# Kernel tuning notes

Hardware: AMD Instinct MI355X
Metric: run time of the kernel (lower is better)

The kernel has to match this reference:

```python
import jax, jax.numpy as jnp
import numpy as np

ATT_HEADS = 4
H_FEATS = 16
IN_FEATS = 64
N_NODES = 50000
N_EDGES = 1000000


def setup_inputs() -> dict:
    key = jax.random.key(0)
    ks = jax.random.split(key, 12)
    h = jax.random.normal(ks[0], (N_NODES, IN_FEATS), dtype=jnp.float32)
    src_idx = jax.random.randint(ks[1], (N_EDGES,), 0, N_NODES)
    dst_idx = jax.random.randint(ks[2], (N_EDGES,), 0, N_NODES)
    s = 1.0 / np.sqrt(IN_FEATS)
    # w_liner: Linear(in_feats, h_feats*att_heads)
    W_w = jax.random.uniform(ks[3], (IN_FEATS, H_FEATS * ATT_HEADS), jnp.float32, -s, s)
    b_w = jax.random.uniform(ks[4], (H_FEATS * ATT_HEADS,), jnp.float32, -s, s)
    # atten: Linear(2*h_feats, 1)
    sa = 1.0 / np.sqrt(2 * H_FEATS)
    W_a = jax.random.uniform(ks[5], (2 * H_FEATS, 1), jnp.float32, -sa, sa)
    b_a = jax.random.uniform(ks[6], (1,), jnp.float32, -sa, sa)
    # relation_aware: d_liner Linear(in_feats, in_feats), f_liner Linear(3*in_feats, 1)
    W_d = jax.random.uniform(ks[7], (IN_FEATS, IN_FEATS), jnp.float32, -s, s)
    b_d = jax.random.uniform(ks[8], (IN_FEATS,), jnp.float32, -s, s)
    sf = 1.0 / np.sqrt(3 * IN_FEATS)
    W_f = jax.random.uniform(ks[9], (3 * IN_FEATS, 1), jnp.float32, -sf, sf)
    b_f = jax.random.uniform(ks[10], (1,), jnp.float32, -sf, sf)
    return {"h": h, "src_idx": src_idx, "dst_idx": dst_idx,
            "W_w": W_w, "b_w": b_w, "W_a": W_a, "b_a": b_a,
            "W_d": W_d, "b_d": b_d, "W_f": W_f, "b_f": b_f}


def reference(h, src_idx, dst_idx, W_w, b_w, W_a, b_a, W_d, b_d, W_f, b_f):
    N = h.shape[0]
    # sign_edges: relation_aware score -> sign per edge
    s_feat = h[src_idx] @ W_d + b_d            # [E, F]
    d_feat = h[dst_idx] @ W_d + b_d            # [E, F]
    e_feat = jnp.concatenate([s_feat, d_feat, s_feat - d_feat], axis=-1)
    score = jnp.tanh(e_feat @ W_f + b_f)[:, 0]  # [E]
    sign = jnp.sign(score)
    # node transform
    hp = h @ W_w + b_w                          # [N, H*hf]
    # message: signed src features, per-head concat with dst, attention logit
    sf = (sign[:, None] * hp[src_idx]).reshape(-1, ATT_HEADS, H_FEATS)  # [E,H,hf]
    df = hp[dst_idx].reshape(-1, ATT_HEADS, H_FEATS)                    # [E,H,hf]
    z = jnp.concatenate([sf, df], axis=-1)                              # [E,H,2hf]
    alpha = jax.nn.leaky_relu(z @ W_a + b_a)                            # [E,H,1]
    # reduce: segment softmax over incoming edges of each dst node
    amax = jax.ops.segment_max(alpha, dst_idx, num_segments=N)          # [N,H,1]
    ex = jnp.exp(alpha - amax[dst_idx])
    esum = jax.ops.segment_sum(ex, dst_idx, num_segments=N)             # [N,H,1]
    w = ex / esum[dst_idx]                                              # [E,H,1]
    out = jax.ops.segment_sum(w * sf, dst_idx, num_segments=N)          # [N,H,hf]
    return out.reshape(N, ATT_HEADS * H_FEATS)
```

## Files before the change

### kernel.cpp

```cpp
#include <hip/hip_runtime.h>
#include <hip/hip_fp16.h>

constexpr int F  = 64;
constexpr int HEADS = 4;
constexpr int CAP = 256;

__global__ __launch_bounds__(256) void node_kernel(
    const float* __restrict__ h,
    const float* __restrict__ W_w, const float* __restrict__ b_w,
    const float* __restrict__ W_a,
    const float* __restrict__ W_d, const float* __restrict__ b_d,
    const float* __restrict__ W_f,
    float* __restrict__ tfeat, __half* __restrict__ hp,
    double* __restrict__ u_arr, double* __restrict__ v_arr,
    float* __restrict__ a_src, float* __restrict__ a_dst,
    unsigned* __restrict__ cnt, int N, int nb)
{
    __shared__ float sWT[F * F];
    __shared__ float sb[F];
    __shared__ double swfA[F], swfB[F];
    __shared__ float sWa[32];

    int tid = threadIdx.x;
    bool isW = blockIdx.x >= nb;
    const float* Wsrc = isW ? W_w : W_d;
    for (int i = tid; i < F * F; i += 256) {
        int k = i >> 6, j = i & 63;
        sWT[j * F + k] = Wsrc[i];
    }
    if (tid < F) sb[tid] = isW ? b_w[tid] : b_d[tid];
    if (!isW && tid < F) {
        swfA[tid] = (double)W_f[tid] + (double)W_f[2 * F + tid];
        swfB[tid] = (double)W_f[F + tid] - (double)W_f[2 * F + tid];
    }
    if (isW && tid < 32) sWa[tid] = W_a[tid];
    __syncthreads();

    int blk = isW ? (blockIdx.x - nb) : blockIdx.x;
    int n = blk * 256 + tid;
    if (n >= N) return;

    if (!isW) cnt[n] = 0;

    float4 hv[16];
    const float4* h4 = reinterpret_cast<const float4*>(h + (size_t)n * F);
#pragma unroll
    for (int i = 0; i < 16; i++) hv[i] = h4[i];

    if (!isW) {
        double u = 0.0, v = 0.0;
        float4 tq;
        float4* trow = reinterpret_cast<float4*>(tfeat + (size_t)n * F);
#pragma unroll 4
        for (int j = 0; j < F; j++) {
            const float4* row = reinterpret_cast<const float4*>(&sWT[j * F]);
            float t = 0.f;
#pragma unroll
            for (int kk = 0; kk < 16; kk++) {
                float4 w = row[kk];
                float4 x = hv[kk];
                t = fmaf(x.x, w.x, t);
                t = fmaf(x.y, w.y, t);
                t = fmaf(x.z, w.z, t);
                t = fmaf(x.w, w.w, t);
            }
            t = t + sb[j];
            u = fma((double)t, swfA[j], u);
            v = fma((double)t, swfB[j], v);
            if ((j & 3) == 0) tq.x = t;
            else if ((j & 3) == 1) tq.y = t;
            else if ((j & 3) == 2) tq.z = t;
            else { tq.w = t; trow[j >> 2] = tq; }
        }
        u_arr[n] = u;
        v_arr[n] = v;
    } else {
        __half2* prow = reinterpret_cast<__half2*>(hp + (size_t)n * F);
#pragma unroll
        for (int qh = 0; qh < 4; qh++) {
            float asq = 0.f, adq = 0.f;
            float pprev = 0.f;
#pragma unroll 4
            for (int jj = 0; jj < 16; jj++) {
                int j = qh * 16 + jj;
                const float4* row = reinterpret_cast<const float4*>(&sWT[j * F]);
                float p = 0.f;
#pragma unroll
                for (int kk = 0; kk < 16; kk++) {
                    float4 w = row[kk];
                    float4 x = hv[kk];
                    p = fmaf(x.x, w.x, p);
                    p = fmaf(x.y, w.y, p);
                    p = fmaf(x.z, w.z, p);
                    p = fmaf(x.w, w.w, p);
                }
                p = p + sb[j];
                asq = fmaf(p, sWa[jj], asq);
                adq = fmaf(p, sWa[16 + jj], adq);
                if ((jj & 1) == 0) pprev = p;
                else prow[j >> 1] = __floats2half2_rn(pprev, p);
            }
            a_src[n * HEADS + qh] = asq;
            a_dst[n * HEADS + qh] = adq;
        }
    }
}

__device__ __noinline__ float tier2_sign(
    const float* __restrict__ tfeat, const float* __restrict__ sWf,
    int s, int d, float bf)
{
    const float4* ts = reinterpret_cast<const float4*>(tfeat + (size_t)s * F);
    const float4* td = reinterpret_cast<const float4*>(tfeat + (size_t)d * F);
    float sv[F];
#pragma unroll
    for (int i = 0; i < 16; i++) {
        float4 a = ts[i];
        sv[4 * i + 0] = a.x; sv[4 * i + 1] = a.y;
        sv[4 * i + 2] = a.z; sv[4 * i + 3] = a.w;
    }
    float acc = 0.f;
#pragma unroll
    for (int j = 0; j < F; j++) acc = fmaf(sv[j], sWf[j], acc);
#pragma unroll
    for (int i = 0; i < 16; i++) {
        float4 a = td[i];
        acc = fmaf(a.x, sWf[F + 4 * i + 0], acc);
        acc = fmaf(a.y, sWf[F + 4 * i + 1], acc);
        acc = fmaf(a.z, sWf[F + 4 * i + 2], acc);
        acc = fmaf(a.w, sWf[F + 4 * i + 3], acc);
    }
#pragma unroll
    for (int i = 0; i < 16; i++) {
        float4 a = td[i];
        acc = fmaf(sv[4 * i + 0] - a.x, sWf[2 * F + 4 * i + 0], acc);
        acc = fmaf(sv[4 * i + 1] - a.y, sWf[2 * F + 4 * i + 1], acc);
        acc = fmaf(sv[4 * i + 2] - a.z, sWf[2 * F + 4 * i + 2], acc);
        acc = fmaf(sv[4 * i + 3] - a.w, sWf[2 * F + 4 * i + 3], acc);
    }
    float sp = acc + bf;
    return (sp > 0.f) ? 1.f : (sp < 0.f ? -1.f : 0.f);
}

__global__ __launch_bounds__(256) void count_sign_kernel(
    const int* __restrict__ src_idx, const int* __restrict__ dst_idx,
    const double* __restrict__ u_arr, const double* __restrict__ v_arr,
    const float* __restrict__ tfeat, const float* __restrict__ W_f,
    const float* __restrict__ b_f,
    unsigned* __restrict__ cnt, unsigned* __restrict__ pc, int E)
{
    __shared__ float sWf[3 * F];
    int tid = threadIdx.x;
    if (tid < 3 * F) sWf[tid] = W_f[tid];
    __syncthreads();

    float bf = b_f[0];
    int e0 = blockIdx.x * 512 + tid;
    int e1 = e0 + 256;
    bool ok0 = e0 < E, ok1 = e1 < E;

    int s0 = 0, d0 = 0, s1 = 0, d1 = 0;
    if (ok0) { s0 = src_idx[e0]; d0 = dst_idx[e0]; }
    if (ok1) { s1 = src_idx[e1]; d1 = dst_idx[e1]; }

    unsigned p0 = ok0 ? atomicAdd(&cnt[d0], 1u) : 0u;
    unsigned p1 = ok1 ? atomicAdd(&cnt[d1], 1u) : 0u;

    double us0 = ok0 ? u_arr[s0] : 0.0, vd0 = ok0 ? v_arr[d0] : 0.0;
    double us1 = ok1 ? u_arr[s1] : 0.0, vd1 = ok1 ? v_arr[d1] : 0.0;
    double m0 = us0 + vd0 + (double)bf;
    double m1 = us1 + vd1 + (double)bf;

    float sg0 = (fabs(m0) >= 1e-4) ? ((m0 > 0.0) ? 1.f : -1.f)
                                   : (ok0 ? tier2_sign(tfeat, sWf, s0, d0, bf) : 0.f);
    float sg1 = (fabs(m1) >= 1e-4) ? ((m1 > 0.0) ? 1.f : -1.f)
                                   : (ok1 ? tier2_sign(tfeat, sWf, s1, d1, bf) : 0.f);

    if (ok0) {
        unsigned c0 = (sg0 > 0.f) ? 0u : (sg0 < 0.f ? 1u : 2u);
        pc[e0] = p0 | (c0 << 30);
    }
    if (ok1) {
        unsigned c1 = (sg1 > 0.f) ? 0u : (sg1 < 0.f ? 1u : 2u);
        pc[e1] = p1 | (c1 << 30);
    }
}

__global__ __launch_bounds__(256) void scan1_kernel(
    const unsigned* __restrict__ cnt, unsigned* __restrict__ rowptr,
    unsigned* __restrict__ bsum, int N)
{
    int t = threadIdx.x;
    int i = blockIdx.x * 256 + t;
    unsigned v = (i < N) ? cnt[i] : 0u;
    unsigned x = v;
#pragma unroll
    for (int off = 1; off < 64; off <<= 1) {
        unsigned y = __shfl_up(x, off);
        if ((t & 63) >= off) x += y;
    }
    __shared__ unsigned wsum[4];
    if ((t & 63) == 63) wsum[t >> 6] = x;
    __syncthreads();
    unsigned pre = 0;
#pragma unroll
    for (int w = 0; w < 3; w++) if (w < (t >> 6)) pre += wsum[w];
    unsigned incl = x + pre;
    if (i < N) rowptr[i] = incl - v;
    if (t == 255) bsum[blockIdx.x] = incl;
}

__global__ __launch_bounds__(256) void scan3_kernel(
    unsigned* __restrict__ rowptr, const unsigned* __restrict__ bsum,
    int N, int E, int nb)
{
    int t = threadIdx.x;
    int lim = min((int)blockIdx.x, nb);
    unsigned v = 0;
    for (int w = t; w < lim; w += 256) v += bsum[w];
#pragma unroll
    for (int off = 32; off >= 1; off >>= 1) v += __shfl_xor(v, off);
    __shared__ unsigned ws[4];
    if ((t & 63) == 0) ws[t >> 6] = v;
    __syncthreads();
    unsigned prefix = ws[0] + ws[1] + ws[2] + ws[3];

    int i = blockIdx.x * 256 + t;
    if (i < N) rowptr[i] += prefix;
    if (i == 0) rowptr[N] = (unsigned)E;
}

__global__ __launch_bounds__(256) void place_kernel(
    const int* __restrict__ src_idx, const int* __restrict__ dst_idx,
    const unsigned* __restrict__ pc, const unsigned* __restrict__ rowptr,
    unsigned* __restrict__ src_packed, int E)
{
    int e = blockIdx.x * 256 + threadIdx.x;
    if (e >= E) return;
    unsigned p = pc[e];
    unsigned pos = p & 0x3FFFFFFFu;
    unsigned code = p & 0xC0000000u;
    int d = dst_idx[e];
    src_packed[rowptr[d] + pos] = (unsigned)src_idx[e] | code;
}

__global__ __launch_bounds__(256) void dst_gather_kernel(
    const unsigned* __restrict__ rowptr,
    const unsigned* __restrict__ src_packed,
    const float* __restrict__ a_src, const float* __restrict__ a_dst,
    const float* __restrict__ b_a,
    const __half* __restrict__ hp,
    float* __restrict__ out, int N)
{
    __shared__ float sw[4][CAP * 4];
    __shared__ unsigned ssrc[4][CAP];

    int tid = threadIdx.x;
    int wslot = tid >> 6;
    int lane = tid & 63;
    int q = lane >> 4;
    int d = (blockIdx.x * 256 + tid) >> 6;
    bool valid = d < N;

    unsigned start = 0, end = 0;
    float ba = b_a[0];
    float4 ad4 = make_float4(0.f, 0.f, 0.f, 0.f);
    if (valid) {
        start = rowptr[d];
        end = rowptr[d + 1];
        ad4 = *reinterpret_cast<const float4*>(a_dst + (size_t)d * HEADS);
    }
    float adq = (q == 0) ? ad4.x : (q == 1) ? ad4.y : (q == 2) ? ad4.z : ad4.w;

    float4 p = make_float4(0.f, 0.f, 0.f, 0.f);
    if (valid) {
        for (unsigned i = start + lane; i < end; i += 64) {
            unsigned sp = src_packed[i];
            unsigned s = sp & 0x3FFFFFFFu;
            unsigned c = sp >> 30;
            float sgn = (c == 0u) ? 1.f : (c == 1u ? -1.f : 0.f);
            float4 as4 = *reinterpret_cast<const float4*>(a_src + (size_t)s * HEADS);
            float ap0 = fmaf(sgn, as4.x, ad4.x) + ba;
            float ap1 = fmaf(sgn, as4.y, ad4.y) + ba;
            float ap2 = fmaf(sgn, as4.z, ad4.z) + ba;
            float ap3 = fmaf(sgn, as4.w, ad4.w) + ba;
            float e0 = expf(ap0 > 0.f ? ap0 : 0.01f * ap0);
            float e1 = expf(ap1 > 0.f ? ap1 : 0.01f * ap1);
            float e2 = expf(ap2 > 0.f ? ap2 : 0.01f * ap2);
            float e3 = expf(ap3 > 0.f ? ap3 : 0.01f * ap3);
            p.x += e0; p.y += e1; p.z += e2; p.w += e3;
            unsigned slot = i - start;
            if (slot < CAP) {
                *reinterpret_cast<float4*>(&sw[wslot][slot * 4]) =
                    make_float4(sgn * e0, sgn * e1, sgn * e2, sgn * e3);
                ssrc[wslot][slot] = s;
            }
        }
    }
    __syncthreads();

#pragma unroll
    for (int off = 32; off >= 1; off >>= 1) {
        p.x += __shfl_xor(p.x, off);
        p.y += __shfl_xor(p.y, off);
        p.z += __shfl_xor(p.z, off);
        p.w += __shfl_xor(p.w, off);
    }
    if (!valid) return;

    float esq = (q == 0) ? p.x : (q == 1) ? p.y : (q == 2) ? p.z : p.w;
    float rinv = (end > start) ? (1.0f / esq) : 0.f;

    const float* swb = &sw[wslot][0];
    const unsigned* ssb = &ssrc[wslot][0];
    unsigned cend = min(end, start + CAP);
    unsigned cnt_c = cend - start;

    float a0 = 0.f, a1 = 0.f, a2 = 0.f, a3 = 0.f;
    unsigned t0 = 0;
    for (; t0 + 8 <= cnt_c; t0 += 8) {
        float w0 = swb[(t0 + 0) * 4 + q], w1 = swb[(t0 + 1) * 4 + q];
        float w2 = swb[(t0 + 2) * 4 + q], w3 = swb[(t0 + 3) * 4 + q];
        float w4 = swb[(t0 + 4) * 4 + q], w5 = swb[(t0 + 5) * 4 + q];
        float w6 = swb[(t0 + 6) * 4 + q], w7 = swb[(t0 + 7) * 4 + q];
        unsigned s0 = ssb[t0 + 0], s1 = ssb[t0 + 1];
        unsigned s2 = ssb[t0 + 2], s3 = ssb[t0 + 3];
        unsigned s4 = ssb[t0 + 4], s5 = ssb[t0 + 5];
        unsigned s6 = ssb[t0 + 6], s7 = ssb[t0 + 7];
        float h0 = __half2float(hp[((size_t)s0 << 6) | (unsigned)lane]);
        float h1 = __half2float(hp[((size_t)s1 << 6) | (unsigned)lane]);
        float h2 = __half2float(hp[((size_t)s2 << 6) | (unsigned)lane]);
        float h3 = __half2float(hp[((size_t)s3 << 6) | (unsigned)lane]);
        float h4 = __half2float(hp[((size_t)s4 << 6) | (unsigned)lane]);
        float h5 = __half2float(hp[((size_t)s5 << 6) | (unsigned)lane]);
        float h6 = __half2float(hp[((size_t)s6 << 6) | (unsigned)lane]);
        float h7 = __half2float(hp[((size_t)s7 << 6) | (unsigned)lane]);
        a0 = fmaf(w0, h0, a0); a1 = fmaf(w1, h1, a1);
        a2 = fmaf(w2, h2, a2); a3 = fmaf(w3, h3, a3);
        a0 = fmaf(w4, h4, a0); a1 = fmaf(w5, h5, a1);
        a2 = fmaf(w6, h6, a2); a3 = fmaf(w7, h7, a3);
    }
    for (; t0 < cnt_c; t0++) {
        float w = swb[t0 * 4 + q];
        unsigned s = ssb[t0];
        a0 = fmaf(w, __half2float(hp[((size_t)s << 6) | (unsigned)lane]), a0);
    }
    for (unsigned i = start + cnt_c; i < end; i++) {
        unsigned sp = src_packed[i];
        unsigned s = sp & 0x3FFFFFFFu;
        unsigned c = sp >> 30;
        float g = (c == 0u) ? 1.f : (c == 1u ? -1.f : 0.f);
        float asv = a_src[s * HEADS + q];
        float ap = fmaf(g, asv, adq) + ba;
        float ev = expf(ap > 0.f ? ap : 0.01f * ap);
        a0 = fmaf(ev * g, __half2float(hp[((size_t)s << 6) | (unsigned)lane]), a0);
    }
    out[((size_t)d << 6) | (unsigned)lane] = ((a0 + a1) + (a2 + a3)) * rinv;
}

extern "C" void kernel_launch(void* const* d_in, const int* in_sizes, int n_in,
                              void* d_out, int out_size, void* d_ws, size_t ws_size,
                              hipStream_t stream)
{
    const float* h       = (const float*)d_in[0];
    const int*   src_idx = (const int*)d_in[1];
    const int*   dst_idx = (const int*)d_in[2];
    const float* W_w     = (const float*)d_in[3];
    const float* b_w     = (const float*)d_in[4];
    const float* W_a     = (const float*)d_in[5];
    const float* b_a     = (const float*)d_in[6];
    const float* W_d     = (const float*)d_in[7];
    const float* b_d     = (const float*)d_in[8];
    const float* W_f     = (const float*)d_in[9];
    const float* b_f     = (const float*)d_in[10];

    int N = in_sizes[0] / F;
    int E = in_sizes[1];
    int nb = (N + 255) / 256;

    char* ws = (char*)d_ws;
    float*    tfeat = (float*)ws;      ws += (size_t)N * F * 4;
    __half*   hp    = (__half*)ws;     ws += (size_t)N * F * 2;
    double*   u_arr = (double*)ws;     ws += (size_t)N * 8;
    double*   v_arr = (double*)ws;     ws += (size_t)N * 8;
    float*    a_src = (float*)ws;      ws += (size_t)N * HEADS * 4;
    float*    a_dst = (float*)ws;      ws += (size_t)N * HEADS * 4;
    unsigned* cnt   = (unsigned*)ws;   ws += (size_t)N * 4;
    unsigned* rowptr= (unsigned*)ws;   ws += ((size_t)N + 4) * 4;
    unsigned* bsum  = (unsigned*)ws;   ws += 1024;
    unsigned* pc    = (unsigned*)ws;   ws += (size_t)E * 4;
    unsigned* src_p = (unsigned*)ws;   ws += (size_t)E * 4;

    float* out = (float*)d_out;

    node_kernel<<<2 * nb, 256, 0, stream>>>(
        h, W_w, b_w, W_a, W_d, b_d, W_f, tfeat, hp, u_arr, v_arr, a_src, a_dst,
        cnt, N, nb);

    count_sign_kernel<<<(E + 511) / 512, 256, 0, stream>>>(
        src_idx, dst_idx, u_arr, v_arr, tfeat, W_f, b_f, cnt, pc, E);

    scan1_kernel<<<nb, 256, 0, stream>>>(cnt, rowptr, bsum, N);
    scan3_kernel<<<nb, 256, 0, stream>>>(rowptr, bsum, N, E, nb);

    place_kernel<<<(E + 255) / 256, 256, 0, stream>>>(
        src_idx, dst_idx, pc, rowptr, src_p, E);

    dst_gather_kernel<<<(N * 64 + 255) / 256, 256, 0, stream>>>(
        rowptr, src_p, a_src, a_dst, b_a, hp, out, N);
}
```

Baseline: 146.7 us.

## Replace CSR scan and placement with fixed-slot per-destination buckets plus overflow list

Drops the two scan kernels and the placement kernel. Each edge now writes its packed source and sign straight into a fixed 64-slot bucket for its destination, using the atomic count as the index, and edges beyond 64 go to a global overflow list. The gather kernel reads the bucket directly and linearly scans the overflow list only for high-degree nodes. The sign-decision inputs u and v also move from double to float, which halves that traffic but may flip signs near the 1e-4 threshold. In exchange the bucket array is sparse (N*64 slots, about 12.8MB) and the overflow scan would be very costly if many nodes exceed 64 in-edges.

Measured after the change: 138.4 us. 1.06x faster.

```diff
diff --git a/kernel.cpp b/kernel.cpp
--- a/kernel.cpp
+++ b/kernel.cpp
@@ -3,7 +3,7 @@
 
 constexpr int F  = 64;
 constexpr int HEADS = 4;
-constexpr int CAP = 256;
+constexpr int K_SLOT = 64;
 
 __global__ __launch_bounds__(256) void node_kernel(
     const float* __restrict__ h,
@@ -12,9 +12,9 @@
     const float* __restrict__ W_d, const float* __restrict__ b_d,
     const float* __restrict__ W_f,
     float* __restrict__ tfeat, __half* __restrict__ hp,
-    double* __restrict__ u_arr, double* __restrict__ v_arr,
+    float* __restrict__ u_arr, float* __restrict__ v_arr,
     float* __restrict__ a_src, float* __restrict__ a_dst,
-    unsigned* __restrict__ cnt, int N, int nb)
+    unsigned* __restrict__ cnt, unsigned* __restrict__ of_cnt, int N, int nb)
 {
     __shared__ float sWT[F * F];
     __shared__ float sb[F];
@@ -34,6 +34,7 @@
         swfB[tid] = (double)W_f[F + tid] - (double)W_f[2 * F + tid];
     }
     if (isW && tid < 32) sWa[tid] = W_a[tid];
+    if (blockIdx.x == 0 && tid == 0) *of_cnt = 0;
     __syncthreads();
 
     int blk = isW ? (blockIdx.x - nb) : blockIdx.x;
@@ -72,8 +73,8 @@
             else if ((j & 3) == 2) tq.z = t;
             else { tq.w = t; trow[j >> 2] = tq; }
         }
-        u_arr[n] = u;
-        v_arr[n] = v;
+        u_arr[n] = (float)u;
+        v_arr[n] = (float)v;
     } else {
         __half2* prow = reinterpret_cast<__half2*>(hp + (size_t)n * F);
 #pragma unroll
@@ -142,12 +143,13 @@
     return (sp > 0.f) ? 1.f : (sp < 0.f ? -1.f : 0.f);
 }
 
-__global__ __launch_bounds__(256) void count_sign_kernel(
+__global__ __launch_bounds__(256) void count_scatter_kernel(
     const int* __restrict__ src_idx, const int* __restrict__ dst_idx,
-    const double* __restrict__ u_arr, const double* __restrict__ v_arr,
+    const float* __restrict__ u_arr, const float* __restrict__ v_arr,
     const float* __restrict__ tfeat, const float* __restrict__ W_f,
     const float* __restrict__ b_f,
-    unsigned* __restrict__ cnt, unsigned* __restrict__ pc, int E)
+    unsigned* __restrict__ cnt, unsigned* __restrict__ slot,
+    unsigned* __restrict__ of_list, unsigned* __restrict__ of_cnt, int E)
 {
     __shared__ float sWf[3 * F];
     int tid = threadIdx.x;
@@ -163,97 +165,52 @@
     if (ok0) { s0 = src_idx[e0]; d0 = dst_idx[e0]; }
     if (ok1) { s1 = src_idx[e1]; d1 = dst_idx[e1]; }
 
+    float us0 = ok0 ? u_arr[s0] : 0.f, vd0 = ok0 ? v_arr[d0] : 0.f;
+    float us1 = ok1 ? u_arr[s1] : 0.f, vd1 = ok1 ? v_arr[d1] : 0.f;
     unsigned p0 = ok0 ? atomicAdd(&cnt[d0], 1u) : 0u;
     unsigned p1 = ok1 ? atomicAdd(&cnt[d1], 1u) : 0u;
 
-    double us0 = ok0 ? u_arr[s0] : 0.0, vd0 = ok0 ? v_arr[d0] : 0.0;
-    double us1 = ok1 ? u_arr[s1] : 0.0, vd1 = ok1 ? v_arr[d1] : 0.0;
-    double m0 = us0 + vd0 + (double)bf;
-    double m1 = us1 + vd1 + (double)bf;
-
-    float sg0 = (fabs(m0) >= 1e-4) ? ((m0 > 0.0) ? 1.f : -1.f)
-                                   : (ok0 ? tier2_sign(tfeat, sWf, s0, d0, bf) : 0.f);
-    float sg1 = (fabs(m1) >= 1e-4) ? ((m1 > 0.0) ? 1.f : -1.f)
-                                   : (ok1 ? tier2_sign(tfeat, sWf, s1, d1, bf) : 0.f);
+    float m0 = us0 + vd0 + bf;
+    float m1 = us1 + vd1 + bf;
+
+    float sg0 = (fabsf(m0) >= 1e-4f) ? ((m0 > 0.f) ? 1.f : -1.f)
+                                     : (ok0 ? tier2_sign(tfeat, sWf, s0, d0, bf) : 0.f);
+    float sg1 = (fabsf(m1) >= 1e-4f) ? ((m1 > 0.f) ? 1.f : -1.f)
+                                     : (ok1 ? tier2_sign(tfeat, sWf, s1, d1, bf) : 0.f);
 
     if (ok0) {
         unsigned c0 = (sg0 > 0.f) ? 0u : (sg0 < 0.f ? 1u : 2u);
-        pc[e0] = p0 | (c0 << 30);
+        unsigned val = (unsigned)s0 | (c0 << 30);
+        if (p0 < (unsigned)K_SLOT) slot[(size_t)d0 * K_SLOT + p0] = val;
+        else {
+            unsigned oi = atomicAdd(of_cnt, 1u);
+            of_list[2 * oi] = (unsigned)d0;
+            of_list[2 * oi + 1] = val;
+        }
     }
     if (ok1) {
         unsigned c1 = (sg1 > 0.f) ? 0u : (sg1 < 0.f ? 1u : 2u);
-        pc[e1] = p1 | (c1 << 30);
-    }
-}
-
-__global__ __launch_bounds__(256) void scan1_kernel(
-    const unsigned* __restrict__ cnt, unsigned* __restrict__ rowptr,
-    unsigned* __restrict__ bsum, int N)
-{
-    int t = threadIdx.x;
-    int i = blockIdx.x * 256 + t;
-    unsigned v = (i < N) ? cnt[i] : 0u;
-    unsigned x = v;
-#pragma unroll
-    for (int off = 1; off < 64; off <<= 1) {
-        unsigned y = __shfl_up(x, off);
-        if ((t & 63) >= off) x += y;
-    }
-    __shared__ unsigned wsum[4];
-    if ((t & 63) == 63) wsum[t >> 6] = x;
-    __syncthreads();
-    unsigned pre = 0;
-#pragma unroll
-    for (int w = 0; w < 3; w++) if (w < (t >> 6)) pre += wsum[w];
-    unsigned incl = x + pre;
-    if (i < N) rowptr[i] = incl - v;
-    if (t == 255) bsum[blockIdx.x] = incl;
-}
-
-__global__ __launch_bounds__(256) void scan3_kernel(
-    unsigned* __restrict__ rowptr, const unsigned* __restrict__ bsum,
-    int N, int E, int nb)
-{
-    int t = threadIdx.x;
-    int lim = min((int)blockIdx.x, nb);
-    unsigned v = 0;
-    for (int w = t; w < lim; w += 256) v += bsum[w];
-#pragma unroll
-    for (int off = 32; off >= 1; off >>= 1) v += __shfl_xor(v, off);
-    __shared__ unsigned ws[4];
-    if ((t & 63) == 0) ws[t >> 6] = v;
-    __syncthreads();
-    unsigned prefix = ws[0] + ws[1] + ws[2] + ws[3];
-
-    int i = blockIdx.x * 256 + t;
-    if (i < N) rowptr[i] += prefix;
-    if (i == 0) rowptr[N] = (unsigned)E;
-}
-
-__global__ __launch_bounds__(256) void place_kernel(
-    const int* __restrict__ src_idx, const int* __restrict__ dst_idx,
-    const unsigned* __restrict__ pc, const unsigned* __restrict__ rowptr,
-    unsigned* __restrict__ src_packed, int E)
-{
-    int e = blockIdx.x * 256 + threadIdx.x;
-    if (e >= E) return;
-    unsigned p = pc[e];
-    unsigned pos = p & 0x3FFFFFFFu;
-    unsigned code = p & 0xC0000000u;
-    int d = dst_idx[e];
-    src_packed[rowptr[d] + pos] = (unsigned)src_idx[e] | code;
+        unsigned val = (unsigned)s1 | (c1 << 30);
+        if (p1 < (unsigned)K_SLOT) slot[(size_t)d1 * K_SLOT + p1] = val;
+        else {
+            unsigned oi = atomicAdd(of_cnt, 1u);
+            of_list[2 * oi] = (unsigned)d1;
+            of_list[2 * oi + 1] = val;
+        }
+    }
 }
 
 __global__ __launch_bounds__(256) void dst_gather_kernel(
-    const unsigned* __restrict__ rowptr,
-    const unsigned* __restrict__ src_packed,
+    const unsigned* __restrict__ cnt,
+    const unsigned* __restrict__ slot,
+    const unsigned* __restrict__ of_list, const unsigned* __restrict__ of_cnt,
     const float* __restrict__ a_src, const float* __restrict__ a_dst,
     const float* __restrict__ b_a,
     const __half* __restrict__ hp,
     float* __restrict__ out, int N)
 {
-    __shared__ float sw[4][CAP * 4];
-    __shared__ unsigned ssrc[4][CAP];
+    __shared__ float sw[4][K_SLOT * 4];
+    __shared__ unsigned ssrc[4][K_SLOT];
 
     int tid = threadIdx.x;
     int wslot = tid >> 6;
@@ -262,38 +219,53 @@
     int d = (blockIdx.x * 256 + tid) >> 6;
     bool valid = d < N;
 
-    unsigned start = 0, end = 0;
+    unsigned deg = 0;
     float ba = b_a[0];
     float4 ad4 = make_float4(0.f, 0.f, 0.f, 0.f);
     if (valid) {
-        start = rowptr[d];
-        end = rowptr[d + 1];
+        deg = cnt[d];
         ad4 = *reinterpret_cast<const float4*>(a_dst + (size_t)d * HEADS);
     }
     float adq = (q == 0) ? ad4.x : (q == 1) ? ad4.y : (q == 2) ? ad4.z : ad4.w;
+    unsigned mdeg = min(deg, (unsigned)K_SLOT);
 
     float4 p = make_float4(0.f, 0.f, 0.f, 0.f);
-    if (valid) {
-        for (unsigned i = start + lane; i < end; i += 64) {
-            unsigned sp = src_packed[i];
-            unsigned s = sp & 0x3FFFFFFFu;
-            unsigned c = sp >> 30;
-            float sgn = (c == 0u) ? 1.f : (c == 1u ? -1.f : 0.f);
-            float4 as4 = *reinterpret_cast<const float4*>(a_src + (size_t)s * HEADS);
-            float ap0 = fmaf(sgn, as4.x, ad4.x) + ba;
-            float ap1 = fmaf(sgn, as4.y, ad4.y) + ba;
-            float ap2 = fmaf(sgn, as4.z, ad4.z) + ba;
-            float ap3 = fmaf(sgn, as4.w, ad4.w) + ba;
-            float e0 = expf(ap0 > 0.f ? ap0 : 0.01f * ap0);
-            float e1 = expf(ap1 > 0.f ? ap1 : 0.01f * ap1);
-            float e2 = expf(ap2 > 0.f ? ap2 : 0.01f * ap2);
-            float e3 = expf(ap3 > 0.f ? ap3 : 0.01f * ap3);
-            p.x += e0; p.y += e1; p.z += e2; p.w += e3;
-            unsigned slot = i - start;
-            if (slot < CAP) {
-                *reinterpret_cast<float4*>(&sw[wslot][slot * 4]) =
-                    make_float4(sgn * e0, sgn * e1, sgn * e2, sgn * e3);
-                ssrc[wslot][slot] = s;
+    if (valid && lane < (int)mdeg) {
+        unsigned sp = slot[(size_t)d * K_SLOT + lane];
+        unsigned s = sp & 0x3FFFFFFFu;
+        unsigned c = sp >> 30;
+        float sgn = (c == 0u) ? 1.f : (c == 1u ? -1.f : 0.f);
+        float4 as4 = *reinterpret_cast<const float4*>(a_src + (size_t)s * HEADS);
+        float ap0 = fmaf(sgn, as4.x, ad4.x) + ba;
+        float ap1 = fmaf(sgn, as4.y, ad4.y) + ba;
+        float ap2 = fmaf(sgn, as4.z, ad4.z) + ba;
+        float ap3 = fmaf(sgn, as4.w, ad4.w) + ba;
+        float e0 = expf(ap0 > 0.f ? ap0 : 0.01f * ap0);
+        float e1 = expf(ap1 > 0.f ? ap1 : 0.01f * ap1);
+        float e2 = expf(ap2 > 0.f ? ap2 : 0.01f * ap2);
+        float e3 = expf(ap3 > 0.f ? ap3 : 0.01f * ap3);
+        p = make_float4(e0, e1, e2, e3);
+        *reinterpret_cast<float4*>(&sw[wslot][lane * 4]) =
+            make_float4(sgn * e0, sgn * e1, sgn * e2, sgn * e3);
+        ssrc[wslot][lane] = s;
+    }
+    if (valid && deg > (unsigned)K_SLOT) {
+        unsigned on = *of_cnt;
+        for (unsigned i = lane; i < on; i += 64) {
+            if (of_list[2 * i] == (unsigned)d) {
+                unsigned sp = of_list[2 * i + 1];
+                unsigned s = sp & 0x3FFFFFFFu;
+                unsigned c = sp >> 30;
+                float sgn = (c == 0u) ? 1.f : (c == 1u ? -1.f : 0.f);
+                float4 as4 = *reinterpret_cast<const float4*>(a_src + (size_t)s * HEADS);
+                float ap0 = fmaf(sgn, as4.x, ad4.x) + ba;
+                float ap1 = fmaf(sgn, as4.y, ad4.y) + ba;
+                float ap2 = fmaf(sgn, as4.z, ad4.z) + ba;
+                float ap3 = fmaf(sgn, as4.w, ad4.w) + ba;
+                p.x += expf(ap0 > 0.f ? ap0 : 0.01f * ap0);
+                p.y += expf(ap1 > 0.f ? ap1 : 0.01f * ap1);
+                p.z += expf(ap2 > 0.f ? ap2 : 0.01f * ap2);
+                p.w += expf(ap3 > 0.f ? ap3 : 0.01f * ap3);
             }
         }
     }
@@ -309,16 +281,14 @@
     if (!valid) return;
 
     float esq = (q == 0) ? p.x : (q == 1) ? p.y : (q == 2) ? p.z : p.w;
-    float rinv = (end > start) ? (1.0f / esq) : 0.f;
+    float rinv = (deg > 0) ? (1.0f / esq) : 0.f;
 
     const float* swb = &sw[wslot][0];
     const unsigned* ssb = &ssrc[wslot][0];
-    unsigned cend = min(end, start + CAP);
-    unsigned cnt_c = cend - start;
 
     float a0 = 0.f, a1 = 0.f, a2 = 0.f, a3 = 0.f;
     unsigned t0 = 0;
-    for (; t0 + 8 <= cnt_c; t0 += 8) {
+    for (; t0 + 8 <= mdeg; t0 += 8) {
         float w0 = swb[(t0 + 0) * 4 + q], w1 = swb[(t0 + 1) * 4 + q];
         float w2 = swb[(t0 + 2) * 4 + q], w3 = swb[(t0 + 3) * 4 + q];
         float w4 = swb[(t0 + 4) * 4 + q], w5 = swb[(t0 + 5) * 4 + q];
@@ -340,20 +310,25 @@
         a0 = fmaf(w4, h4, a0); a1 = fmaf(w5, h5, a1);
         a2 = fmaf(w6, h6, a2); a3 = fmaf(w7, h7, a3);
     }
-    for (; t0 < cnt_c; t0++) {
+    for (; t0 < mdeg; t0++) {
         float w = swb[t0 * 4 + q];
         unsigned s = ssb[t0];
         a0 = fmaf(w, __half2float(hp[((size_t)s << 6) | (unsigned)lane]), a0);
     }
-    for (unsigned i = start + cnt_c; i < end; i++) {
-        unsigned sp = src_packed[i];
-        unsigned s = sp & 0x3FFFFFFFu;
-        unsigned c = sp >> 30;
-        float g = (c == 0u) ? 1.f : (c == 1u ? -1.f : 0.f);
-        float asv = a_src[s * HEADS + q];
-        float ap = fmaf(g, asv, adq) + ba;
-        float ev = expf(ap > 0.f ? ap : 0.01f * ap);
-        a0 = fmaf(ev * g, __half2float(hp[((size_t)s << 6) | (unsigned)lane]), a0);
+    if (deg > (unsigned)K_SLOT) {
+        unsigned on = *of_cnt;
+        for (unsigned i = 0; i < on; i++) {
+            if (of_list[2 * i] == (unsigned)d) {
+                unsigned sp = of_list[2 * i + 1];
+                unsigned s = sp & 0x3FFFFFFFu;
+                unsigned c = sp >> 30;
+                float g = (c == 0u) ? 1.f : (c == 1u ? -1.f : 0.f);
+                float asv = a_src[s * HEADS + q];
+                float ap = fmaf(g, asv, adq) + ba;
+                float ev = expf(ap > 0.f ? ap : 0.01f * ap);
+                a0 = fmaf(ev * g, __half2float(hp[((size_t)s << 6) | (unsigned)lane]), a0);
+            }
+        }
     }
     out[((size_t)d << 6) | (unsigned)lane] = ((a0 + a1) + (a2 + a3)) * rinv;
 }
@@ -379,33 +354,27 @@
     int nb = (N + 255) / 256;
 
     char* ws = (char*)d_ws;
-    float*    tfeat = (float*)ws;      ws += (size_t)N * F * 4;
-    __half*   hp    = (__half*)ws;     ws += (size_t)N * F * 2;
-    double*   u_arr = (double*)ws;     ws += (size_t)N * 8;
-    double*   v_arr = (double*)ws;     ws += (size_t)N * 8;
-    float*    a_src = (float*)ws;      ws += (size_t)N * HEADS * 4;
-    float*    a_dst = (float*)ws;      ws += (size_t)N * HEADS * 4;
-    unsigned* cnt   = (unsigned*)ws;   ws += (size_t)N * 4;
-    unsigned* rowptr= (unsigned*)ws;   ws += ((size_t)N + 4) * 4;
-    unsigned* bsum  = (unsigned*)ws;   ws += 1024;
-    unsigned* pc    = (unsigned*)ws;   ws += (size_t)E * 4;
-    unsigned* src_p = (unsigned*)ws;   ws += (size_t)E * 4;
+    float*    tfeat  = (float*)ws;     ws += (size_t)N * F * 4;
+    __half*   hp     = (__half*)ws;    ws += (size_t)N * F * 2;
+    float*    u_arr  = (float*)ws;     ws += (size_t)N * 4;
+    float*    v_arr  = (float*)ws;     ws += (size_t)N * 4;
+    float*    a_src  = (float*)ws;     ws += (size_t)N * HEADS * 4;
+    float*    a_dst  = (float*)ws;     ws += (size_t)N * HEADS * 4;
+    unsigned* cnt    = (unsigned*)ws;  ws += (size_t)N * 4;
+    unsigned* of_cnt = (unsigned*)ws;  ws += 64;
+    unsigned* slot   = (unsigned*)ws;  ws += (size_t)N * K_SLOT * 4;
+    unsigned* of_list= (unsigned*)ws;  ws += (size_t)E * 8;
 
     float* out = (float*)d_out;
 
     node_kernel<<<2 * nb, 256, 0, stream>>>(
         h, W_w, b_w, W_a, W_d, b_d, W_f, tfeat, hp, u_arr, v_arr, a_src, a_dst,
-        cnt, N, nb);
-
-    count_sign_kernel<<<(E + 511) / 512, 256, 0, stream>>>(
-        src_idx, dst_idx, u_arr, v_arr, tfeat, W_f, b_f, cnt, pc, E);
-
-    scan1_kernel<<<nb, 256, 0, stream>>>(cnt, rowptr, bsum, N);
-    scan3_kernel<<<nb, 256, 0, stream>>>(rowptr, bsum, N, E, nb);
-
-    place_kernel<<<(E + 255) / 256, 256, 0, stream>>>(
-        src_idx, dst_idx, pc, rowptr, src_p, E);
+        cnt, of_cnt, N, nb);
+
+    count_scatter_kernel<<<(E + 511) / 512, 256, 0, stream>>>(
+        src_idx, dst_idx, u_arr, v_arr, tfeat, W_f, b_f,
+        cnt, slot, of_list, of_cnt, E);
 
     dst_gather_kernel<<<(N * 64 + 255) / 256, 256, 0, stream>>>(
-        rowptr, src_p, a_src, a_dst, b_a, hp, out, N);
-}
+        cnt, slot, of_list, of_cnt, a_src, a_dst, b_a, hp, out, N);
+}
```
